# Performance work log

Measured on AMD Instinct MI355X. Metric: run time of the kernel, lower is better.

## Reference

```python
import jax, jax.numpy as jnp
import numpy as np

# NF4 codebook (bitsandbytes quant_type='nf4'), 16 fixed quantile values
NF4 = jnp.array([
    -1.0, -0.6961928009986877, -0.5250730514526367, -0.39491748809814453,
    -0.28444138169288635, -0.18477343022823334, -0.09105003625154495, 0.0,
    0.07958029955625534, 0.16093020141124725, 0.24611230194568634,
    0.33791524171829224, 0.44070982933044434, 0.5626170039176941,
    0.7229568362236023, 1.0], dtype=jnp.float32)
BLK = 64  # bnb default blocksize for nf4


def dequant_nf4(codes, absmax):
    # codes: [out, in] int codes in [0,16); absmax: [out, in//BLK] blockwise scale
    out_f, in_f = codes.shape
    w = NF4[codes].reshape(out_f, in_f // BLK, BLK) * absmax[:, :, None]
    return w.reshape(out_f, in_f)


def setup_inputs() -> dict:
    key = jax.random.key(0)
    ks = jax.random.split(key, 7)
    hd, m, T = 4096, 14336, 2048
    x = jax.random.normal(ks[0], (T, hd), dtype=jnp.float32)
    gate_codes = jax.random.randint(ks[1], (m, hd), 0, 16, dtype=jnp.int32)
    gate_absmax = jax.random.uniform(ks[2], (m, hd // BLK), dtype=jnp.float32) * 0.05
    up_codes = jax.random.randint(ks[3], (m, hd), 0, 16, dtype=jnp.int32)
    up_absmax = jax.random.uniform(ks[4], (m, hd // BLK), dtype=jnp.float32) * 0.05
    down_codes = jax.random.randint(ks[5], (hd, m), 0, 16, dtype=jnp.int32)
    down_absmax = jax.random.uniform(ks[6], (hd, m // BLK), dtype=jnp.float32) * 0.05
    return {"x": x, "gate_codes": gate_codes, "gate_absmax": gate_absmax,
            "up_codes": up_codes, "up_absmax": up_absmax,
            "down_codes": down_codes, "down_absmax": down_absmax}


def reference(x, gate_codes, gate_absmax, up_codes, up_absmax, down_codes, down_absmax):
    # SwiGLU MLP: down( silu(gate(x)) * up(x) ), weights dequantized from nf4
    Wg = dequant_nf4(gate_codes, gate_absmax)   # [m, hd]
    Wu = dequant_nf4(up_codes, up_absmax)       # [m, hd]
    Wd = dequant_nf4(down_codes, down_absmax)   # [hd, m]
    g = x @ Wg.T                                # [T, m]
    h = jax.nn.silu(g) * (x @ Wu.T)             # [T, m]
    return h @ Wd.T                             # [T, hd]
```

## Files before the change

kernel.cpp:

```cpp
#include <hip/hip_runtime.h>
#include <hip/hip_bf16.h>
#include <cstdint>
#include <cstddef>

#define TDIM 2048
#define HDIM 4096
#define MDIM 14336

typedef __attribute__((ext_vector_type(8))) __bf16 bf16x8;
typedef __attribute__((ext_vector_type(4))) float f32x4;

__device__ __constant__ float NF4_LUT[16] = {
    -1.0f, -0.6961928009986877f, -0.5250730514526367f, -0.39491748809814453f,
    -0.28444138169288635f, -0.18477343022823334f, -0.09105003625154495f, 0.0f,
    0.07958029955625534f, 0.16093020141124725f, 0.24611230194568634f,
    0.33791524171829224f, 0.44070982933044434f, 0.5626170039176941f,
    0.7229568362236023f, 1.0f};

__device__ inline void g2l16(const void* g, void* l) {
  __builtin_amdgcn_global_load_lds(
      (const __attribute__((address_space(1))) unsigned int*)g,
      (__attribute__((address_space(3))) unsigned int*)l,
      16 , 0, 0);
}

__global__ __launch_bounds__(256) void f32_to_bf16_k(
    const float* __restrict__ in, __hip_bfloat16* __restrict__ out, int n8) {
  for (int i = blockIdx.x * 256 + threadIdx.x; i < n8; i += gridDim.x * 256) {
    const float4* p = (const float4*)(in + (size_t)i * 8);
    float4 a = p[0], b = p[1];
    union { __hip_bfloat16 h[8]; int4 v; } u;
    u.h[0] = __float2bfloat16(a.x);
    u.h[1] = __float2bfloat16(a.y);
    u.h[2] = __float2bfloat16(a.z);
    u.h[3] = __float2bfloat16(a.w);
    u.h[4] = __float2bfloat16(b.x);
    u.h[5] = __float2bfloat16(b.y);
    u.h[6] = __float2bfloat16(b.z);
    u.h[7] = __float2bfloat16(b.w);
    *(int4*)(out + (size_t)i * 8) = u.v;
  }
}

__global__ __launch_bounds__(256) void dequant_nf4_k(
    const int* __restrict__ codes, const float* __restrict__ absmax,
    __hip_bfloat16* __restrict__ W, int K) {
  __shared__ float lut[16];
  if (threadIdx.x < 16) lut[threadIdx.x] = NF4_LUT[threadIdx.x];
  __syncthreads();
  const int row = blockIdx.x;
  const int K8 = K >> 3;
  const size_t rbase = (size_t)row * K;
  for (int c8 = threadIdx.x; c8 < K8; c8 += 256) {
    const int col = c8 << 3;
    const float am = absmax[(size_t)row * (K >> 6) + (col >> 6)];
    const int4* cp = (const int4*)(codes + rbase + col);
    int4 ca = cp[0], cb = cp[1];
    union { __hip_bfloat16 h[8]; int4 v; } u;
    u.h[0] = __float2bfloat16(lut[ca.x & 15] * am);
    u.h[1] = __float2bfloat16(lut[ca.y & 15] * am);
    u.h[2] = __float2bfloat16(lut[ca.z & 15] * am);
    u.h[3] = __float2bfloat16(lut[ca.w & 15] * am);
    u.h[4] = __float2bfloat16(lut[cb.x & 15] * am);
    u.h[5] = __float2bfloat16(lut[cb.y & 15] * am);
    u.h[6] = __float2bfloat16(lut[cb.z & 15] * am);
    u.h[7] = __float2bfloat16(lut[cb.w & 15] * am);
    *(int4*)(W + rbase + col) = u.v;
  }
}

template <int EPI>
__global__ __launch_bounds__(256, 2) void gemm_nt_k(
    const __hip_bfloat16* __restrict__ A, const __hip_bfloat16* __restrict__ B,
    void* __restrict__ Cv, const __hip_bfloat16* __restrict__ Gin,
    int M, int N, int K) {
  __shared__ __align__(16) char sA[128 * 128];
  __shared__ __align__(16) char sB[128 * 128];

  const int tid = threadIdx.x;
  const int lane = tid & 63;
  const int wid = tid >> 6;

  const int nbn = N >> 7;
  const int nwg = (M >> 7) * nbn;
  const int cpx = nwg >> 3;
  const int bid = blockIdx.x;
  const int wg = (bid & 7) * cpx + (bid >> 3);
  const int bm = wg / nbn, bn = wg % nbn;

  const int srow = lane >> 3;
  const int scolb = ((lane & 7) ^ srow) << 4;
  const char* gA = (const char*)A +
      ((size_t)(bm * 128 + wid * 8 + srow) * K) * 2 + scolb;
  const char* gB = (const char*)B +
      ((size_t)(bn * 128 + wid * 8 + srow) * K) * 2 + scolb;
  const size_t cstep = (size_t)64 * K;
  char* lA = sA + wid * 1024;
  char* lB = sB + wid * 1024;

  const int wm = wid >> 1, wn = wid & 1;
  const int colsw = (((lane >> 4) << 4) ^ ((lane & 7) << 4));
  const int aoff = (wm * 64 + (lane & 15)) * 128 + colsw;
  const int boff = (wn * 64 + (lane & 15)) * 128 + colsw;

  f32x4 acc[4][4] = {};

  const int nk = K >> 6;
  for (int kt = 0; kt < nk; ++kt) {
    const char* pa = gA + (size_t)kt * 128;
    const char* pb = gB + (size_t)kt * 128;
#pragma unroll
    for (int c = 0; c < 4; ++c) {
      g2l16(pa + c * cstep, lA + c * 4096);
      g2l16(pb + c * cstep, lB + c * 4096);
    }
    __syncthreads();
#pragma unroll
    for (int ks = 0; ks < 2; ++ks) {
      bf16x8 af[4], bfr[4];
#pragma unroll
      for (int i = 0; i < 4; ++i) {
        af[i] = *(const bf16x8*)(sA + ((aoff + i * 2048) ^ (ks << 6)));
        bfr[i] = *(const bf16x8*)(sB + ((boff + i * 2048) ^ (ks << 6)));
      }
#pragma unroll
      for (int mi = 0; mi < 4; ++mi)
#pragma unroll
        for (int nj = 0; nj < 4; ++nj)
          acc[mi][nj] = __builtin_amdgcn_mfma_f32_16x16x32_bf16(
              af[mi], bfr[nj], acc[mi][nj], 0, 0, 0);
    }
    __syncthreads();
  }

  const int row0 = bm * 128 + wm * 64 + ((lane >> 4) << 2);
  const int col0 = bn * 128 + wn * 64 + (lane & 15);
#pragma unroll
  for (int mi = 0; mi < 4; ++mi) {
#pragma unroll
    for (int nj = 0; nj < 4; ++nj) {
#pragma unroll
      for (int r = 0; r < 4; ++r) {
        const size_t idx =
            (size_t)(row0 + mi * 16 + r) * N + (col0 + nj * 16);
        const float v = acc[mi][nj][r];
        if (EPI == 0) {
          ((__hip_bfloat16*)Cv)[idx] = __float2bfloat16(v);
        } else if (EPI == 1) {
          const float g = __bfloat162float(Gin[idx]);
          const float h = g / (1.0f + __expf(-g)) * v;
          ((__hip_bfloat16*)Cv)[idx] = __float2bfloat16(h);
        } else {
          ((float*)Cv)[idx] = v;
        }
      }
    }
  }
}

extern "C" void kernel_launch(void* const* d_in, const int* in_sizes, int n_in,
                              void* d_out, int out_size, void* d_ws,
                              size_t ws_size, hipStream_t stream) {
  const float* x = (const float*)d_in[0];
  const int* gate_codes = (const int*)d_in[1];
  const float* gate_absmax = (const float*)d_in[2];
  const int* up_codes = (const int*)d_in[3];
  const float* up_absmax = (const float*)d_in[4];
  const int* down_codes = (const int*)d_in[5];
  const float* down_absmax = (const float*)d_in[6];

  char* ws = (char*)d_ws;
  __hip_bfloat16* xb = (__hip_bfloat16*)ws;
  __hip_bfloat16* Wb =
      (__hip_bfloat16*)(ws + (size_t)TDIM * HDIM * 2);
  __hip_bfloat16* Hb =
      (__hip_bfloat16*)(ws + (size_t)TDIM * HDIM * 2 +
                        (size_t)MDIM * HDIM * 2);

  f32_to_bf16_k<<<2048, 256, 0, stream>>>(x, xb, (TDIM * HDIM) / 8);

  dequant_nf4_k<<<MDIM, 256, 0, stream>>>(gate_codes, gate_absmax, Wb, HDIM);
  gemm_nt_k<0><<<(TDIM / 128) * (MDIM / 128), 256, 0, stream>>>(
      xb, Wb, Hb, nullptr, TDIM, MDIM, HDIM);

  dequant_nf4_k<<<MDIM, 256, 0, stream>>>(up_codes, up_absmax, Wb, HDIM);
  gemm_nt_k<1><<<(TDIM / 128) * (MDIM / 128), 256, 0, stream>>>(
      xb, Wb, Hb, Hb, TDIM, MDIM, HDIM);

  dequant_nf4_k<<<HDIM, 256, 0, stream>>>(down_codes, down_absmax, Wb, MDIM);
  gemm_nt_k<2><<<(TDIM / 128) * (HDIM / 128), 256, 0, stream>>>(
      Hb, Wb, (float*)d_out, nullptr, TDIM, HDIM, MDIM);
}
```

Measured before the change: 1.061 ms.

## Replace GEMM with 256x256 8-wave double-buffered pipelined kernel and split-K down projection

Replaces the 128x128 single-buffered GEMM with a 256x256 tile, 512-thread kernel that double-buffers 128KB of LDS and interleaves async global-to-LDS loads with MFMA phases, using explicit vmcnt waits, barriers and setprio. The aim is to hide load latency and raise reuse per tile, cutting the memory-bound stalls of the old load-sync-compute loop. The down projection uses split-K by 2 with float atomicAdd into an output zeroed by memset, to fill the GPU despite fewer output tiles. Atomics make the summation order nondeterministic and add a memset, and the large LDS footprint limits occupancy.

```diff
diff --git a/kernel.cpp b/kernel.cpp
--- a/kernel.cpp
+++ b/kernel.cpp
@@ -17,11 +17,10 @@
     0.33791524171829224f, 0.44070982933044434f, 0.5626170039176941f,
     0.7229568362236023f, 1.0f};
 
-__device__ inline void g2l16(const void* g, void* l) {
+__device__ __forceinline__ void g2l16(const void* g, void* l) {
   __builtin_amdgcn_global_load_lds(
       (const __attribute__((address_space(1))) unsigned int*)g,
-      (__attribute__((address_space(3))) unsigned int*)l,
-      16 , 0, 0);
+      (__attribute__((address_space(3))) unsigned int*)l, 16, 0, 0);
 }
 
 __global__ __launch_bounds__(256) void f32_to_bf16_k(
@@ -69,89 +68,149 @@
   }
 }
 
+template <int B_, int MH, int NH, int VM, typename F>
+__device__ __forceinline__ void phase8(const char* aRd, const char* bRd,
+                                       f32x4 (&acc)[8][4], F&& stage) {
+  bf16x8 af[4][2], bv[2][2];
+  const char* ab = aRd + B_ * 32768 + MH * 16384;
+  const char* bb = bRd + B_ * 32768 + NH * 16384;
+#pragma unroll
+  for (int q = 0; q < 4; ++q) {
+    af[q][0] = *(const bf16x8*)((uintptr_t)(ab + q * 2048));
+    af[q][1] = *(const bf16x8*)((uintptr_t)(ab + q * 2048) ^ 64);
+  }
+#pragma unroll
+  for (int j = 0; j < 2; ++j) {
+    bv[j][0] = *(const bf16x8*)((uintptr_t)(bb + j * 2048));
+    bv[j][1] = *(const bf16x8*)((uintptr_t)(bb + j * 2048) ^ 64);
+  }
+  stage();
+  if (VM == 4) asm volatile("s_waitcnt vmcnt(4)" ::: "memory");
+  if (VM == 0) asm volatile("s_waitcnt vmcnt(0)" ::: "memory");
+  asm volatile("" ::: "memory");
+  __builtin_amdgcn_s_barrier();
+  asm volatile("" ::: "memory");
+  __builtin_amdgcn_s_setprio(1);
+#pragma unroll
+  for (int q = 0; q < 4; ++q)
+#pragma unroll
+    for (int j = 0; j < 2; ++j) {
+      acc[MH * 4 + q][NH * 2 + j] = __builtin_amdgcn_mfma_f32_16x16x32_bf16(
+          af[q][0], bv[j][0], acc[MH * 4 + q][NH * 2 + j], 0, 0, 0);
+      acc[MH * 4 + q][NH * 2 + j] = __builtin_amdgcn_mfma_f32_16x16x32_bf16(
+          af[q][1], bv[j][1], acc[MH * 4 + q][NH * 2 + j], 0, 0, 0);
+    }
+  __builtin_amdgcn_s_setprio(0);
+  asm volatile("" ::: "memory");
+  __builtin_amdgcn_s_barrier();
+  asm volatile("" ::: "memory");
+}
+
 template <int EPI>
-__global__ __launch_bounds__(256, 2) void gemm_nt_k(
+__global__ __launch_bounds__(512, 2) void gemm8_nt_k(
     const __hip_bfloat16* __restrict__ A, const __hip_bfloat16* __restrict__ B,
     void* __restrict__ Cv, const __hip_bfloat16* __restrict__ Gin,
-    int M, int N, int K) {
-  __shared__ __align__(16) char sA[128 * 128];
-  __shared__ __align__(16) char sB[128 * 128];
+    int M, int N, int Kfull, int Kloc, int ksplit) {
+  __shared__ __align__(16) char lds[131072];
 
   const int tid = threadIdx.x;
   const int lane = tid & 63;
   const int wid = tid >> 6;
-
-  const int nbn = N >> 7;
-  const int nwg = (M >> 7) * nbn;
-  const int cpx = nwg >> 3;
+  const int wm = wid >> 2, wn = wid & 3;
+
+  const int nbn = N >> 8;
+  const int nwg2 = (M >> 8) * nbn;
+  const int G = nwg2 * ksplit;
+  const int q8 = G >> 3;
   const int bid = blockIdx.x;
-  const int wg = (bid & 7) * cpx + (bid >> 3);
-  const int bm = wg / nbn, bn = wg % nbn;
+  const int wg = (bid & 7) * q8 + (bid >> 3);
+  const int kh = wg / nwg2;
+  const int rem = wg - kh * nwg2;
+  const int bm = rem / nbn;
+  const int bn = rem - bm * nbn;
+
+  const size_t Kb = (size_t)Kfull * 2;
+  const size_t koffb = (size_t)kh * Kloc * 2;
 
   const int srow = lane >> 3;
-  const int scolb = ((lane & 7) ^ srow) << 4;
-  const char* gA = (const char*)A +
-      ((size_t)(bm * 128 + wid * 8 + srow) * K) * 2 + scolb;
-  const char* gB = (const char*)B +
-      ((size_t)(bn * 128 + wid * 8 + srow) * K) * 2 + scolb;
-  const size_t cstep = (size_t)64 * K;
-  char* lA = sA + wid * 1024;
-  char* lB = sB + wid * 1024;
-
-  const int wm = wid >> 1, wn = wid & 1;
+  const int scw = ((lane & 7) ^ srow) << 4;
+  const uint8_t* gA = (const uint8_t*)A +
+      (size_t)(bm * 256 + wid * 8 + srow) * Kb + koffb + scw;
+  const uint8_t* gB = (const uint8_t*)B +
+      (size_t)(bn * 256 + wid * 8 + srow) * Kb + koffb + scw;
+  char* ldsw = lds + wid * 1024;
+
+  auto stageA = [&](int h, int b, int tt) {
+    const uint8_t* g = gA + (size_t)(h * 128) * Kb + (size_t)tt * 128;
+    char* l = ldsw + b * 32768 + h * 16384;
+    g2l16(g, l);
+    g2l16(g + 64 * Kb, l + 8192);
+  };
+  auto stageB = [&](int h, int b, int tt) {
+    const uint8_t* g = gB + (size_t)(h * 128) * Kb + (size_t)tt * 128;
+    char* l = ldsw + 65536 + b * 32768 + h * 16384;
+    g2l16(g, l);
+    g2l16(g + 64 * Kb, l + 8192);
+  };
+
   const int colsw = (((lane >> 4) << 4) ^ ((lane & 7) << 4));
-  const int aoff = (wm * 64 + (lane & 15)) * 128 + colsw;
-  const int boff = (wn * 64 + (lane & 15)) * 128 + colsw;
-
-  f32x4 acc[4][4] = {};
-
-  const int nk = K >> 6;
-  for (int kt = 0; kt < nk; ++kt) {
-    const char* pa = gA + (size_t)kt * 128;
-    const char* pb = gB + (size_t)kt * 128;
-#pragma unroll
-    for (int c = 0; c < 4; ++c) {
-      g2l16(pa + c * cstep, lA + c * 4096);
-      g2l16(pb + c * cstep, lB + c * 4096);
-    }
-    __syncthreads();
-#pragma unroll
-    for (int ks = 0; ks < 2; ++ks) {
-      bf16x8 af[4], bfr[4];
-#pragma unroll
-      for (int i = 0; i < 4; ++i) {
-        af[i] = *(const bf16x8*)(sA + ((aoff + i * 2048) ^ (ks << 6)));
-        bfr[i] = *(const bf16x8*)(sB + ((boff + i * 2048) ^ (ks << 6)));
-      }
-#pragma unroll
-      for (int mi = 0; mi < 4; ++mi)
-#pragma unroll
-        for (int nj = 0; nj < 4; ++nj)
-          acc[mi][nj] = __builtin_amdgcn_mfma_f32_16x16x32_bf16(
-              af[mi], bfr[nj], acc[mi][nj], 0, 0, 0);
-    }
-    __syncthreads();
-  }
-
-  const int row0 = bm * 128 + wm * 64 + ((lane >> 4) << 2);
-  const int col0 = bn * 128 + wn * 64 + (lane & 15);
-#pragma unroll
-  for (int mi = 0; mi < 4; ++mi) {
-#pragma unroll
-    for (int nj = 0; nj < 4; ++nj) {
+  const char* aRd = lds + (wm * 64 + (lane & 15)) * 128 + colsw;
+  const char* bRd = lds + 65536 + (wn * 32 + (lane & 15)) * 128 + colsw;
+
+  f32x4 acc[8][4] = {};
+
+  const int nt = Kloc >> 6;
+  const int niter = nt >> 1;
+
+  stageA(0, 0, 0); stageA(1, 0, 0); stageB(0, 0, 0); stageB(1, 0, 0);
+  stageA(0, 1, 1); stageB(0, 1, 1);
+  asm volatile("s_waitcnt vmcnt(4)" ::: "memory");
+  __builtin_amdgcn_s_barrier();
+  asm volatile("" ::: "memory");
+
+  for (int i = 0; i < niter - 1; ++i) {
+    const int t = i * 2;
+    phase8<0, 0, 0, -1>(aRd, bRd, acc, [&] { stageA(1, 1, t + 1); });
+    phase8<0, 0, 1, -1>(aRd, bRd, acc, [&] { stageB(1, 1, t + 1); });
+    phase8<0, 1, 0, -1>(aRd, bRd, acc, [&] { stageA(0, 0, t + 2); });
+    phase8<0, 1, 1,  4>(aRd, bRd, acc, [&] { stageB(0, 0, t + 2); });
+    phase8<1, 0, 0, -1>(aRd, bRd, acc, [&] { stageA(1, 0, t + 2); });
+    phase8<1, 0, 1, -1>(aRd, bRd, acc, [&] { stageB(1, 0, t + 2); });
+    phase8<1, 1, 0, -1>(aRd, bRd, acc, [&] { stageA(0, 1, t + 3); });
+    phase8<1, 1, 1,  4>(aRd, bRd, acc, [&] { stageB(0, 1, t + 3); });
+  }
+  {
+    const int t = nt - 2;
+    phase8<0, 0, 0, -1>(aRd, bRd, acc, [&] { stageA(1, 1, t + 1); });
+    phase8<0, 0, 1, -1>(aRd, bRd, acc, [&] { stageB(1, 1, t + 1); });
+    phase8<0, 1, 0, -1>(aRd, bRd, acc, [&] {});
+    phase8<0, 1, 1,  0>(aRd, bRd, acc, [&] {});
+    phase8<1, 0, 0, -1>(aRd, bRd, acc, [&] {});
+    phase8<1, 0, 1, -1>(aRd, bRd, acc, [&] {});
+    phase8<1, 1, 0, -1>(aRd, bRd, acc, [&] {});
+    phase8<1, 1, 1, -1>(aRd, bRd, acc, [&] {});
+  }
+
+#pragma unroll
+  for (int mi = 0; mi < 8; ++mi) {
+    const int grow0 = bm * 256 + (mi >> 2) * 128 + wm * 64 + (mi & 3) * 16 +
+                      ((lane >> 4) << 2);
+#pragma unroll
+    for (int ni = 0; ni < 4; ++ni) {
+      const int gcol = bn * 256 + (ni >> 1) * 128 + wn * 32 + (ni & 1) * 16 +
+                       (lane & 15);
 #pragma unroll
       for (int r = 0; r < 4; ++r) {
-        const size_t idx =
-            (size_t)(row0 + mi * 16 + r) * N + (col0 + nj * 16);
-        const float v = acc[mi][nj][r];
+        const size_t idx = (size_t)(grow0 + r) * N + gcol;
+        const float v = acc[mi][ni][r];
         if (EPI == 0) {
           ((__hip_bfloat16*)Cv)[idx] = __float2bfloat16(v);
         } else if (EPI == 1) {
           const float g = __bfloat162float(Gin[idx]);
-          const float h = g / (1.0f + __expf(-g)) * v;
-          ((__hip_bfloat16*)Cv)[idx] = __float2bfloat16(h);
+          ((__hip_bfloat16*)Cv)[idx] =
+              __float2bfloat16(g / (1.0f + __expf(-g)) * v);
         } else {
-          ((float*)Cv)[idx] = v;
+          atomicAdd(&((float*)Cv)[idx], v);
         }
       }
     }
@@ -171,23 +230,21 @@
 
   char* ws = (char*)d_ws;
   __hip_bfloat16* xb = (__hip_bfloat16*)ws;
-  __hip_bfloat16* Wb =
-      (__hip_bfloat16*)(ws + (size_t)TDIM * HDIM * 2);
-  __hip_bfloat16* Hb =
-      (__hip_bfloat16*)(ws + (size_t)TDIM * HDIM * 2 +
-                        (size_t)MDIM * HDIM * 2);
+  __hip_bfloat16* Wb = (__hip_bfloat16*)(ws + (size_t)TDIM * HDIM * 2);
+  __hip_bfloat16* Hb = (__hip_bfloat16*)(ws + (size_t)TDIM * HDIM * 2 +
+                                         (size_t)MDIM * HDIM * 2);
+
+  hipMemsetAsync(d_out, 0, (size_t)TDIM * HDIM * 4, stream);
 
   f32_to_bf16_k<<<2048, 256, 0, stream>>>(x, xb, (TDIM * HDIM) / 8);
 
   dequant_nf4_k<<<MDIM, 256, 0, stream>>>(gate_codes, gate_absmax, Wb, HDIM);
-  gemm_nt_k<0><<<(TDIM / 128) * (MDIM / 128), 256, 0, stream>>>(
-      xb, Wb, Hb, nullptr, TDIM, MDIM, HDIM);
-
+  gemm8_nt_k<0><<<(TDIM / 256) * (MDIM / 256), 512, 0, stream>>>(
+      xb, Wb, Hb, nullptr, TDIM, MDIM, HDIM, HDIM, 1);
   dequant_nf4_k<<<MDIM, 256, 0, stream>>>(up_codes, up_absmax, Wb, HDIM);
-  gemm_nt_k<1><<<(TDIM / 128) * (MDIM / 128), 256, 0, stream>>>(
-      xb, Wb, Hb, Hb, TDIM, MDIM, HDIM);
-
+  gemm8_nt_k<1><<<(TDIM / 256) * (MDIM / 256), 512, 0, stream>>>(
+      xb, Wb, Hb, Hb, TDIM, MDIM, HDIM, HDIM, 1);
   dequant_nf4_k<<<HDIM, 256, 0, stream>>>(down_codes, down_absmax, Wb, MDIM);
-  gemm_nt_k<2><<<(TDIM / 128) * (HDIM / 128), 256, 0, stream>>>(
-      Hb, Wb, (float*)d_out, nullptr, TDIM, HDIM, MDIM);
-}
+  gemm8_nt_k<2><<<2 * (TDIM / 256) * (HDIM / 256), 512, 0, stream>>>(
+      Hb, Wb, (float*)d_out, nullptr, TDIM, HDIM, MDIM, MDIM / 2, 2);
+}
```

Result: slower. 1.859 ms (+75.3%).

## Use 256x128 tiles with 8 waves and split-K the down GEMM with atomics

Applied to the files above, without the earlier changes.

The GEMM kernel now runs 512 threads per block and covers a 256x128 output tile, with the eight waves sharing each loaded B tile. The down projection, which has few output tiles, is split along K into two halves that accumulate into a zeroed fp32 output with atomicAdd. This targets better B reuse and more parallelism on the down GEMM. The cost is larger LDS use, launch bounds of 512 threads with a hint of 4 blocks, an extra memset, and atomic traffic that can make the output order-dependent.

```diff
diff --git a/kernel.cpp b/kernel.cpp
--- a/kernel.cpp
+++ b/kernel.cpp
@@ -17,11 +17,10 @@
     0.33791524171829224f, 0.44070982933044434f, 0.5626170039176941f,
     0.7229568362236023f, 1.0f};
 
-__device__ inline void g2l16(const void* g, void* l) {
+__device__ __forceinline__ void g2l16(const void* g, void* l) {
   __builtin_amdgcn_global_load_lds(
       (const __attribute__((address_space(1))) unsigned int*)g,
-      (__attribute__((address_space(3))) unsigned int*)l,
-      16 , 0, 0);
+      (__attribute__((address_space(3))) unsigned int*)l, 16, 0, 0);
 }
 
 __global__ __launch_bounds__(256) void f32_to_bf16_k(
@@ -70,70 +69,76 @@
 }
 
 template <int EPI>
-__global__ __launch_bounds__(256, 2) void gemm_nt_k(
+__global__ __launch_bounds__(512, 4) void gemm97_nt_k(
     const __hip_bfloat16* __restrict__ A, const __hip_bfloat16* __restrict__ B,
     void* __restrict__ Cv, const __hip_bfloat16* __restrict__ Gin,
-    int M, int N, int K) {
-  __shared__ __align__(16) char sA[128 * 128];
+    int M, int N, int Kfull, int Kloc, int ksplit) {
+  __shared__ __align__(16) char sA[256 * 128];
   __shared__ __align__(16) char sB[128 * 128];
 
   const int tid = threadIdx.x;
   const int lane = tid & 63;
   const int wid = tid >> 6;
+  const int wm = wid >> 1, wn = wid & 1;
 
   const int nbn = N >> 7;
-  const int nwg = (M >> 7) * nbn;
-  const int cpx = nwg >> 3;
+  const int nwg2 = (M >> 8) * nbn;
+  const int G = nwg2 * ksplit;
+  const int q8 = G >> 3;
   const int bid = blockIdx.x;
-  const int wg = (bid & 7) * cpx + (bid >> 3);
-  const int bm = wg / nbn, bn = wg % nbn;
+  const int wg = (bid & 7) * q8 + (bid >> 3);
+  const int kh = wg / nwg2;
+  const int rem = wg - kh * nwg2;
+  const int bm = rem / nbn;
+  const int bn = rem - bm * nbn;
+
+  const size_t Kb = (size_t)Kfull * 2;
+  const size_t koffb = (size_t)kh * Kloc * 2;
 
   const int srow = lane >> 3;
-  const int scolb = ((lane & 7) ^ srow) << 4;
-  const char* gA = (const char*)A +
-      ((size_t)(bm * 128 + wid * 8 + srow) * K) * 2 + scolb;
-  const char* gB = (const char*)B +
-      ((size_t)(bn * 128 + wid * 8 + srow) * K) * 2 + scolb;
-  const size_t cstep = (size_t)64 * K;
+  const int scw = ((lane & 7) ^ srow) << 4;
+  const uint8_t* gA = (const uint8_t*)A +
+      (size_t)(bm * 256 + wid * 8 + srow) * Kb + koffb + scw;
+  const uint8_t* gB = (const uint8_t*)B +
+      (size_t)(bn * 128 + wid * 8 + srow) * Kb + koffb + scw;
   char* lA = sA + wid * 1024;
   char* lB = sB + wid * 1024;
 
-  const int wm = wid >> 1, wn = wid & 1;
   const int colsw = (((lane >> 4) << 4) ^ ((lane & 7) << 4));
-  const int aoff = (wm * 64 + (lane & 15)) * 128 + colsw;
-  const int boff = (wn * 64 + (lane & 15)) * 128 + colsw;
+  const char* aRd = sA + (wm * 64 + (lane & 15)) * 128 + colsw;
+  const char* bRd = sB + (wn * 64 + (lane & 15)) * 128 + colsw;
 
   f32x4 acc[4][4] = {};
 
-  const int nk = K >> 6;
-  for (int kt = 0; kt < nk; ++kt) {
-    const char* pa = gA + (size_t)kt * 128;
-    const char* pb = gB + (size_t)kt * 128;
+  const int nt = Kloc >> 6;
+  for (int kt = 0; kt < nt; ++kt) {
+    const size_t kb = (size_t)kt * 128;
 #pragma unroll
-    for (int c = 0; c < 4; ++c) {
-      g2l16(pa + c * cstep, lA + c * 4096);
-      g2l16(pb + c * cstep, lB + c * 4096);
-    }
+    for (int s = 0; s < 4; ++s)
+      g2l16(gA + (size_t)(s * 64) * Kb + kb, lA + s * 8192);
+#pragma unroll
+    for (int s = 0; s < 2; ++s)
+      g2l16(gB + (size_t)(s * 64) * Kb + kb, lB + s * 8192);
     __syncthreads();
 #pragma unroll
     for (int ks = 0; ks < 2; ++ks) {
-      bf16x8 af[4], bfr[4];
+      bf16x8 af[4], bv[4];
 #pragma unroll
       for (int i = 0; i < 4; ++i) {
-        af[i] = *(const bf16x8*)(sA + ((aoff + i * 2048) ^ (ks << 6)));
-        bfr[i] = *(const bf16x8*)(sB + ((boff + i * 2048) ^ (ks << 6)));
+        af[i] = *(const bf16x8*)((uintptr_t)(aRd + i * 2048) ^ (ks << 6));
+        bv[i] = *(const bf16x8*)((uintptr_t)(bRd + i * 2048) ^ (ks << 6));
       }
 #pragma unroll
       for (int mi = 0; mi < 4; ++mi)
 #pragma unroll
         for (int nj = 0; nj < 4; ++nj)
           acc[mi][nj] = __builtin_amdgcn_mfma_f32_16x16x32_bf16(
-              af[mi], bfr[nj], acc[mi][nj], 0, 0, 0);
+              af[mi], bv[nj], acc[mi][nj], 0, 0, 0);
     }
     __syncthreads();
   }
 
-  const int row0 = bm * 128 + wm * 64 + ((lane >> 4) << 2);
+  const int row0 = bm * 256 + wm * 64 + ((lane >> 4) << 2);
   const int col0 = bn * 128 + wn * 64 + (lane & 15);
 #pragma unroll
   for (int mi = 0; mi < 4; ++mi) {
@@ -148,10 +153,10 @@
           ((__hip_bfloat16*)Cv)[idx] = __float2bfloat16(v);
         } else if (EPI == 1) {
           const float g = __bfloat162float(Gin[idx]);
-          const float h = g / (1.0f + __expf(-g)) * v;
-          ((__hip_bfloat16*)Cv)[idx] = __float2bfloat16(h);
+          ((__hip_bfloat16*)Cv)[idx] =
+              __float2bfloat16(g / (1.0f + __expf(-g)) * v);
         } else {
-          ((float*)Cv)[idx] = v;
+          atomicAdd(&((float*)Cv)[idx], v);
         }
       }
     }
@@ -171,23 +176,21 @@
 
   char* ws = (char*)d_ws;
   __hip_bfloat16* xb = (__hip_bfloat16*)ws;
-  __hip_bfloat16* Wb =
-      (__hip_bfloat16*)(ws + (size_t)TDIM * HDIM * 2);
-  __hip_bfloat16* Hb =
-      (__hip_bfloat16*)(ws + (size_t)TDIM * HDIM * 2 +
-                        (size_t)MDIM * HDIM * 2);
+  __hip_bfloat16* Wb = (__hip_bfloat16*)(ws + (size_t)TDIM * HDIM * 2);
+  __hip_bfloat16* Hb = (__hip_bfloat16*)(ws + (size_t)TDIM * HDIM * 2 +
+                                         (size_t)MDIM * HDIM * 2);
+
+  hipMemsetAsync(d_out, 0, (size_t)TDIM * HDIM * 4, stream);
 
   f32_to_bf16_k<<<2048, 256, 0, stream>>>(x, xb, (TDIM * HDIM) / 8);
 
   dequant_nf4_k<<<MDIM, 256, 0, stream>>>(gate_codes, gate_absmax, Wb, HDIM);
-  gemm_nt_k<0><<<(TDIM / 128) * (MDIM / 128), 256, 0, stream>>>(
-      xb, Wb, Hb, nullptr, TDIM, MDIM, HDIM);
-
+  gemm97_nt_k<0><<<(TDIM / 256) * (MDIM / 128), 512, 0, stream>>>(
+      xb, Wb, Hb, nullptr, TDIM, MDIM, HDIM, HDIM, 1);
   dequant_nf4_k<<<MDIM, 256, 0, stream>>>(up_codes, up_absmax, Wb, HDIM);
-  gemm_nt_k<1><<<(TDIM / 128) * (MDIM / 128), 256, 0, stream>>>(
-      xb, Wb, Hb, Hb, TDIM, MDIM, HDIM);
-
+  gemm97_nt_k<1><<<(TDIM / 256) * (MDIM / 128), 512, 0, stream>>>(
+      xb, Wb, Hb, Hb, TDIM, MDIM, HDIM, HDIM, 1);
   dequant_nf4_k<<<HDIM, 256, 0, stream>>>(down_codes, down_absmax, Wb, MDIM);
-  gemm_nt_k<2><<<(TDIM / 128) * (HDIM / 128), 256, 0, stream>>>(
-      Hb, Wb, (float*)d_out, nullptr, TDIM, HDIM, MDIM);
+  gemm97_nt_k<2><<<2 * (TDIM / 256) * (HDIM / 128), 512, 0, stream>>>(
+      Hb, Wb, (float*)d_out, nullptr, TDIM, HDIM, MDIM, MDIM / 2, 2);
 }
```

Result: slower. 1.133 ms (+6.8%).

## Add 256x256 eight-wave pipelined GEMM for the up projection with SiLU epilogue

Applied to the files above, without the earlier changes.

Replaces the 128x128 single-buffered GEMM used for the up projection (with its fused SiLU-gate multiply) by a new 512-thread kernel. It computes a 256x256 tile per block, double-buffers LDS, and interleaves global-to-LDS staging with MFMA work through explicit vmcnt waits, barriers and setprio. The aim is higher data reuse per loaded tile and hiding of load latency behind the matrix math. In exchange it uses 128KB of LDS, so only one block fits per CU, and the hand-written wait counts must stay correct. The gate and down GEMMs are left on the old kernel.

```diff
diff --git a/kernel.cpp b/kernel.cpp
--- a/kernel.cpp
+++ b/kernel.cpp
@@ -9,6 +9,14 @@
 
 typedef __attribute__((ext_vector_type(8))) __bf16 bf16x8;
 typedef __attribute__((ext_vector_type(4))) float f32x4;
+
+#define VMW(n) asm volatile("s_waitcnt vmcnt(" #n ")" ::: "memory")
+#define BARR                                  \
+  do {                                        \
+    asm volatile("" ::: "memory");            \
+    __builtin_amdgcn_s_barrier();             \
+    asm volatile("" ::: "memory");            \
+  } while (0)
 
 __device__ __constant__ float NF4_LUT[16] = {
     -1.0f, -0.6961928009986877f, -0.5250730514526367f, -0.39491748809814453f,
@@ -17,11 +25,10 @@
     0.33791524171829224f, 0.44070982933044434f, 0.5626170039176941f,
     0.7229568362236023f, 1.0f};
 
-__device__ inline void g2l16(const void* g, void* l) {
+__device__ __forceinline__ void g2l16(const void* g, void* l) {
   __builtin_amdgcn_global_load_lds(
       (const __attribute__((address_space(1))) unsigned int*)g,
-      (__attribute__((address_space(3))) unsigned int*)l,
-      16 , 0, 0);
+      (__attribute__((address_space(3))) unsigned int*)l, 16, 0, 0);
 }
 
 __global__ __launch_bounds__(256) void f32_to_bf16_k(
@@ -146,13 +153,188 @@
         const float v = acc[mi][nj][r];
         if (EPI == 0) {
           ((__hip_bfloat16*)Cv)[idx] = __float2bfloat16(v);
-        } else if (EPI == 1) {
-          const float g = __bfloat162float(Gin[idx]);
-          const float h = g / (1.0f + __expf(-g)) * v;
-          ((__hip_bfloat16*)Cv)[idx] = __float2bfloat16(h);
         } else {
           ((float*)Cv)[idx] = v;
         }
+      }
+    }
+  }
+}
+
+#define LDA8(dst, B_, H_)                                                     \
+  _Pragma("unroll") for (int q = 0; q < 4; ++q) {                             \
+    dst[q][0] = *(const bf16x8*)((uintptr_t)(aRd + (B_)*32768 +               \
+                                             (H_)*16384 + q * 2048));         \
+    dst[q][1] = *(const bf16x8*)(((uintptr_t)(aRd + (B_)*32768 +              \
+                                              (H_)*16384 + q * 2048)) ^ 64);  \
+  }
+#define LDB4(dst, B_, H_)                                                     \
+  _Pragma("unroll") for (int j = 0; j < 2; ++j) {                             \
+    dst[j][0] = *(const bf16x8*)((uintptr_t)(bRd + (B_)*32768 +               \
+                                             (H_)*16384 + j * 2048));         \
+    dst[j][1] = *(const bf16x8*)(((uintptr_t)(bRd + (B_)*32768 +              \
+                                              (H_)*16384 + j * 2048)) ^ 64);  \
+  }
+#define MFMA16(AF, BV, MH, NH)                                                \
+  __builtin_amdgcn_s_setprio(1);                                              \
+  _Pragma("unroll") for (int q = 0; q < 4; ++q)                               \
+  _Pragma("unroll") for (int j = 0; j < 2; ++j) {                             \
+    acc[(MH)*4 + q][(NH)*2 + j] = __builtin_amdgcn_mfma_f32_16x16x32_bf16(    \
+        AF[q][0], BV[j][0], acc[(MH)*4 + q][(NH)*2 + j], 0, 0, 0);            \
+    acc[(MH)*4 + q][(NH)*2 + j] = __builtin_amdgcn_mfma_f32_16x16x32_bf16(    \
+        AF[q][1], BV[j][1], acc[(MH)*4 + q][(NH)*2 + j], 0, 0, 0);            \
+  }                                                                           \
+  __builtin_amdgcn_s_setprio(0)
+
+__global__ __launch_bounds__(512, 1) void up_gemm8_k(
+    const __hip_bfloat16* __restrict__ A, const __hip_bfloat16* __restrict__ B,
+    __hip_bfloat16* __restrict__ Cv, const __hip_bfloat16* __restrict__ Gin,
+    int M, int N, int K) {
+  __shared__ __align__(16) char lds[131072];
+
+  const int tid = threadIdx.x;
+  const int lane = tid & 63;
+  const int wid = tid >> 6;
+  const int wm = wid >> 2, wn = wid & 3;
+
+  const int nbn = N >> 8;
+  const int nwg = (M >> 8) * nbn;
+  const int q8 = nwg >> 3;
+  const int bid = blockIdx.x;
+  const int wg = (bid & 7) * q8 + (bid >> 3);
+  const int bm = wg / nbn;
+  const int bn = wg - bm * nbn;
+
+  const size_t Kb = (size_t)K * 2;
+
+  const int srow = lane >> 3;
+  const int scw = ((lane & 7) ^ srow) << 4;
+  const uint8_t* gA = (const uint8_t*)A +
+      (size_t)(bm * 256 + wid * 8 + srow) * Kb + scw;
+  const uint8_t* gB = (const uint8_t*)B +
+      (size_t)(bn * 256 + wid * 8 + srow) * Kb + scw;
+  char* ldsw = lds + wid * 1024;
+
+  auto stageA = [&](int h, int b, int tt) {
+    const uint8_t* g = gA + (size_t)(h * 128) * Kb + (size_t)tt * 128;
+    char* l = ldsw + b * 32768 + h * 16384;
+    g2l16(g, l);
+    g2l16(g + 64 * Kb, l + 8192);
+  };
+  auto stageB = [&](int h, int b, int tt) {
+    const uint8_t* g = gB + (size_t)(h * 128) * Kb + (size_t)tt * 128;
+    char* l = ldsw + 65536 + b * 32768 + h * 16384;
+    g2l16(g, l);
+    g2l16(g + 64 * Kb, l + 8192);
+  };
+
+  const int colsw = (((lane >> 4) << 4) ^ ((lane & 7) << 4));
+  const char* aRd = lds + (wm * 64 + (lane & 15)) * 128 + colsw;
+  const char* bRd = lds + 65536 + (wn * 32 + (lane & 15)) * 128 + colsw;
+
+  f32x4 acc[8][4] = {};
+  bf16x8 afA[4][2], afB[4][2], bv0A[2][2], bv0B[2][2], bv1[2][2];
+
+  const int nt = K >> 6;
+  const int niter = nt >> 1;
+
+  stageA(0, 0, 0); stageB(0, 0, 0); stageA(1, 0, 0); stageB(1, 0, 0);
+  stageA(0, 1, 1); stageB(0, 1, 1);
+  VMW(8);
+  BARR;
+  LDA8(afA, 0, 0);
+  LDB4(bv0A, 0, 0);
+
+  for (int i = 0; i < niter - 1; ++i) {
+    const int t = i * 2;
+    VMW(4); BARR;
+    LDB4(bv1, 0, 1);
+    stageA(1, 1, t + 1);
+    MFMA16(afA, bv0A, 0, 0);
+    BARR;
+    BARR;
+    LDA8(afB, 0, 1);
+    stageB(1, 1, t + 1);
+    MFMA16(afA, bv1, 0, 1);
+    BARR;
+    BARR;
+    stageA(0, 0, t + 2);
+    MFMA16(afB, bv1, 1, 1);
+    BARR;
+    VMW(6); BARR;
+    LDA8(afA, 1, 0);
+    LDB4(bv0B, 1, 0);
+    stageB(0, 0, t + 2);
+    MFMA16(afB, bv0A, 1, 0);
+    BARR;
+    VMW(4); BARR;
+    LDB4(bv1, 1, 1);
+    stageA(1, 0, t + 2);
+    MFMA16(afA, bv0B, 0, 0);
+    BARR;
+    BARR;
+    LDA8(afB, 1, 1);
+    stageB(1, 0, t + 2);
+    MFMA16(afA, bv1, 0, 1);
+    BARR;
+    BARR;
+    stageA(0, 1, t + 3);
+    MFMA16(afB, bv1, 1, 1);
+    BARR;
+    VMW(6); BARR;
+    LDA8(afA, 0, 0);
+    LDB4(bv0A, 0, 0);
+    stageB(0, 1, t + 3);
+    MFMA16(afB, bv0B, 1, 0);
+    BARR;
+  }
+  {
+    VMW(4); BARR;
+    LDB4(bv1, 0, 1);
+    stageA(1, 1, nt - 1);
+    MFMA16(afA, bv0A, 0, 0);
+    BARR;
+    BARR;
+    LDA8(afB, 0, 1);
+    stageB(1, 1, nt - 1);
+    MFMA16(afA, bv1, 0, 1);
+    BARR;
+    BARR;
+    MFMA16(afB, bv1, 1, 1);
+    BARR;
+    VMW(4); BARR;
+    LDA8(afA, 1, 0);
+    LDB4(bv0B, 1, 0);
+    MFMA16(afB, bv0A, 1, 0);
+    BARR;
+    VMW(0); BARR;
+    LDB4(bv1, 1, 1);
+    MFMA16(afA, bv0B, 0, 0);
+    BARR;
+    BARR;
+    LDA8(afB, 1, 1);
+    MFMA16(afA, bv1, 0, 1);
+    BARR;
+    BARR;
+    MFMA16(afB, bv1, 1, 1);
+    BARR;
+    BARR;
+    MFMA16(afB, bv0B, 1, 0);
+  }
+
+#pragma unroll
+  for (int mi = 0; mi < 8; ++mi) {
+    const int grow0 = bm * 256 + (mi >> 2) * 128 + wm * 64 + (mi & 3) * 16 +
+                      ((lane >> 4) << 2);
+#pragma unroll
+    for (int ni = 0; ni < 4; ++ni) {
+      const int gcol = bn * 256 + (ni >> 1) * 128 + wn * 32 + (ni & 1) * 16 +
+                       (lane & 15);
+#pragma unroll
+      for (int r = 0; r < 4; ++r) {
+        const size_t idx = (size_t)(grow0 + r) * N + gcol;
+        const float g = __bfloat162float(Gin[idx]);
+        Cv[idx] = __float2bfloat16(g / (1.0f + __expf(-g)) * acc[mi][ni][r]);
       }
     }
   }
@@ -171,22 +353,18 @@
 
   char* ws = (char*)d_ws;
   __hip_bfloat16* xb = (__hip_bfloat16*)ws;
-  __hip_bfloat16* Wb =
-      (__hip_bfloat16*)(ws + (size_t)TDIM * HDIM * 2);
-  __hip_bfloat16* Hb =
-      (__hip_bfloat16*)(ws + (size_t)TDIM * HDIM * 2 +
-                        (size_t)MDIM * HDIM * 2);
+  __hip_bfloat16* Wb = (__hip_bfloat16*)(ws + (size_t)TDIM * HDIM * 2);
+  __hip_bfloat16* Hb = (__hip_bfloat16*)(ws + (size_t)TDIM * HDIM * 2 +
+                                         (size_t)MDIM * HDIM * 2);
 
   f32_to_bf16_k<<<2048, 256, 0, stream>>>(x, xb, (TDIM * HDIM) / 8);
 
   dequant_nf4_k<<<MDIM, 256, 0, stream>>>(gate_codes, gate_absmax, Wb, HDIM);
   gemm_nt_k<0><<<(TDIM / 128) * (MDIM / 128), 256, 0, stream>>>(
       xb, Wb, Hb, nullptr, TDIM, MDIM, HDIM);
-
   dequant_nf4_k<<<MDIM, 256, 0, stream>>>(up_codes, up_absmax, Wb, HDIM);
-  gemm_nt_k<1><<<(TDIM / 128) * (MDIM / 128), 256, 0, stream>>>(
+  up_gemm8_k<<<(TDIM / 256) * (MDIM / 256), 512, 0, stream>>>(
       xb, Wb, Hb, Hb, TDIM, MDIM, HDIM);
-
   dequant_nf4_k<<<HDIM, 256, 0, stream>>>(down_codes, down_absmax, Wb, MDIM);
   gemm_nt_k<2><<<(TDIM / 128) * (HDIM / 128), 256, 0, stream>>>(
       Hb, Wb, (float*)d_out, nullptr, TDIM, HDIM, MDIM);
```

After: 1.648 ms. 1.55x slower.
